# Kernel optimization log

Hardware: AMD Instinct MI355X
Metric: run time of the kernel (lower is better)

The kernel has to match this reference:

```python
import jax, jax.numpy as jnp
from jax import lax
import numpy as np


def conv2d(x, w, b):
    # x: NCHW, w: OIHW, VALID padding, stride 1
    y = lax.conv_general_dilated(x, w, (1, 1), 'VALID',
                                 dimension_numbers=('NCHW', 'OIHW', 'NCHW'))
    return y + b[None, :, None, None]


def prelu(x, a):
    # per-channel PReLU, a: (C,)
    return jnp.where(x >= 0, x, a[None, :, None, None] * x)


def maxpool_ceil(x, k, s):
    # max pool with ceil_mode=True: pad right/bottom with -inf as needed
    H, W = x.shape[2], x.shape[3]
    def pad_amt(n):
        out = -(-(n - k) // s) + 1  # ceil
        return max(0, (out - 1) * s + k - n)
    ph, pw = pad_amt(H), pad_amt(W)
    return lax.reduce_window(x, -jnp.inf, lax.max,
                             (1, 1, k, k), (1, 1, s, s),
                             ((0, 0), (0, 0), (0, ph), (0, pw)))


def setup_inputs() -> dict:
    key = jax.random.key(0)
    ks = jax.random.split(key, 24)
    N = 2048
    x = jax.random.normal(ks[0], (N, 3, 48, 48), dtype=jnp.float32)

    def w_init(k, shape, fan_in):
        return jax.random.normal(k, shape, dtype=jnp.float32) * (1.0 / np.sqrt(fan_in))

    inp = {'x': x}
    inp['c1w'] = w_init(ks[1], (32, 3, 3, 3), 3 * 9)
    inp['c1b'] = jnp.zeros((32,), jnp.float32)
    inp['a1'] = jax.random.uniform(ks[2], (32,), jnp.float32, 0.1, 0.4)
    inp['c2w'] = w_init(ks[3], (64, 32, 3, 3), 32 * 9)
    inp['c2b'] = jnp.zeros((64,), jnp.float32)
    inp['a2'] = jax.random.uniform(ks[4], (64,), jnp.float32, 0.1, 0.4)
    inp['c3w'] = w_init(ks[5], (64, 64, 3, 3), 64 * 9)
    inp['c3b'] = jnp.zeros((64,), jnp.float32)
    inp['a3'] = jax.random.uniform(ks[6], (64,), jnp.float32, 0.1, 0.4)
    inp['c4w'] = w_init(ks[7], (128, 64, 2, 2), 64 * 4)
    inp['c4b'] = jnp.zeros((128,), jnp.float32)
    inp['a4'] = jax.random.uniform(ks[8], (128,), jnp.float32, 0.1, 0.4)
    inp['d5w'] = w_init(ks[9], (256, 1152), 1152)
    inp['d5b'] = jnp.zeros((256,), jnp.float32)
    inp['a5'] = jax.random.uniform(ks[10], (256,), jnp.float32, 0.1, 0.4)
    inp['d61w'] = w_init(ks[11], (2, 256), 256)
    inp['d61b'] = jnp.zeros((2,), jnp.float32)
    inp['d62w'] = w_init(ks[12], (4, 256), 256)
    inp['d62b'] = jnp.zeros((4,), jnp.float32)
    inp['d63w'] = w_init(ks[13], (10, 256), 256)
    inp['d63b'] = jnp.zeros((10,), jnp.float32)
    return inp


def reference(x, c1w, c1b, a1, c2w, c2b, a2, c3w, c3b, a3, c4w, c4b, a4,
              d5w, d5b, a5, d61w, d61b, d62w, d62b, d63w, d63b):
    h = prelu(conv2d(x, c1w, c1b), a1)          # [N,32,46,46]
    h = maxpool_ceil(h, 3, 2)                   # [N,32,23,23]
    h = prelu(conv2d(h, c2w, c2b), a2)          # [N,64,21,21]
    h = maxpool_ceil(h, 3, 2)                   # [N,64,10,10]
    h = prelu(conv2d(h, c3w, c3b), a3)          # [N,64,8,8]
    h = maxpool_ceil(h, 2, 2)                   # [N,64,4,4]
    h = prelu(conv2d(h, c4w, c4b), a4)          # [N,128,3,3]
    # torch: x.permute(0,3,2,1).contiguous().view(N,-1)
    h = jnp.transpose(h, (0, 3, 2, 1)).reshape(h.shape[0], -1)  # [N,1152]
    h = h @ d5w.T + d5b                         # [N,256]
    h = jnp.where(h >= 0, h, a5 * h)            # PReLU over features
    a = jax.nn.softmax(h @ d61w.T + d61b, axis=1)  # class probs [N,2]
    b = h @ d62w.T + d62b
    c = h @ d63w.T + d63b                       # landmarks [N,10]
    return (b, c, a)
```

## Files before the change

### kernel.cpp

```cpp
#include <hip/hip_runtime.h>
#include <hip/hip_bf16.h>
#include <hip/hip_fp16.h>
#include <stdint.h>

typedef short s16x8 __attribute__((ext_vector_type(8)));
typedef unsigned short u16x8 __attribute__((ext_vector_type(8)));
typedef _Float16 f16x8 __attribute__((ext_vector_type(8)));
typedef float f32x4 __attribute__((ext_vector_type(4)));

__device__ __forceinline__ unsigned short f2bf(float f) {
    union { float f; unsigned u; } v; v.f = f;
    unsigned u = v.u;
    unsigned r = u + 0x7fffu + ((u >> 16) & 1u);
    return (unsigned short)(r >> 16);
}
__device__ __forceinline__ float bf2f(unsigned short h) {
    union { unsigned u; float f; } v; v.u = ((unsigned)h) << 16;
    return v.f;
}
__device__ __forceinline__ unsigned pkbf(float a, float b) {
    __hip_bfloat162 h = __float22bfloat162_rn(float2{a, b});
    union { __hip_bfloat162 h; unsigned u; } c; c.h = h; return c.u;
}
__device__ __forceinline__ float lo2f(unsigned d) {
    union { unsigned u; float f; } v; v.u = d << 16; return v.f;
}
__device__ __forceinline__ float hi2f(unsigned d) {
    union { unsigned u; float f; } v; v.u = d & 0xffff0000u; return v.f;
}
__device__ __forceinline__ unsigned short f2h(float f) {
    __half h = __float2half(f);
    union { __half h; unsigned short u; } c; c.h = h; return c.u;
}

__global__ void k0_prep(const float* __restrict__ c2w, const float* __restrict__ c3w,
                        const float* __restrict__ c4w, const float* __restrict__ d5w,
                        unsigned short* __restrict__ w2, unsigned short* __restrict__ w3,
                        unsigned short* __restrict__ w4, unsigned short* __restrict__ w5) {
    int t = blockIdx.x * 256 + threadIdx.x;
    if (t < 18432) {
        int kpos = t / 2048, rem = t % 2048, oc = rem / 32, ic = rem % 32;
        w2[t] = f2bf(c2w[(oc * 32 + ic) * 9 + kpos]);
        return;
    }
    t -= 18432;
    if (t < 36864) {
        int kpos = t / 4096, rem = t % 4096, oc = rem / 64, ic = rem % 64;
        w3[t] = f2bf(c3w[(oc * 64 + ic) * 9 + kpos]);
        return;
    }
    t -= 36864;
    if (t < 32768) {
        int kpos = t / 8192, rem = t % 8192, oc = rem / 64, ic = rem % 64;
        w4[t] = f2bf(c4w[(oc * 64 + ic) * 4 + kpos]);
        return;
    }
    t -= 32768;
    if (t < 294912) w5[t] = f2bf(d5w[t]);
}

__global__ __launch_bounds__(256, 6)
void k1_conv1(const float* __restrict__ x, const float* __restrict__ c1w,
              const float* __restrict__ c1b, const float* __restrict__ a1,
              unsigned short* __restrict__ p1) {
    __shared__ unsigned short xstrip[1008];
    __shared__ unsigned short cbuf[230 * 40];
    __shared__ unsigned short wlds[1024];
    __shared__ float bls[32], als[32];

    const int n = blockIdx.x, tid = threadIdx.x;
    const int w = tid >> 6, lane = tid & 63, q = lane >> 4, l16 = lane & 15;

    for (int t = tid; t < 1024; t += 256) {
        int oc = t >> 5, k = t & 31;
        wlds[t] = (k < 27) ? f2h(c1w[oc * 27 + k]) : (unsigned short)0;
    }
    if (tid < 32) { bls[tid] = c1b[tid]; als[tid] = a1[tid]; }
    __syncthreads();

    f16x8 Wf[2];
    #pragma unroll
    for (int nt = 0; nt < 2; ++nt) {
        union { u16x8 u; f16x8 f; } cc;
        cc.u = *(const u16x8*)(wlds + (nt * 16 + l16) * 32 + q * 8);
        Wf[nt] = cc.f;
    }

    float bq[2][4], aq[2][4];
    #pragma unroll
    for (int nt = 0; nt < 2; ++nt)
    #pragma unroll
    for (int r = 0; r < 4; ++r) {
        bq[nt][r] = bls[nt * 16 + q * 4 + r];
        aq[nt][r] = als[nt * 16 + q * 4 + r];
    }

    int off[8];
    #pragma unroll
    for (int j = 0; j < 8; ++j) {
        int k = q * 8 + j;
        int kk = k < 27 ? k : 26;
        int ic = kk / 9, r9 = kk - ic * 9, ky = r9 / 3, kx = r9 - ky * 3;
        off[j] = ic * 336 + ky * 48 + kx;
    }

    auto do_pool = [&](int sp, int nprows, int kymax) {
        int ntask = nprows * 92;
        int t = tid;
        if (t < ntask) {
            int ocg = t & 3; unsigned r2 = (unsigned)t >> 2;
            int px = (int)(r2 % 23u), py_l = (int)(r2 / 23u);
            int kxmax = (px == 22) ? 2 : 3;
            int base = (2 * py_l * 46 + 2 * px) * 40 + ocg * 8;
            float m0 = -3e38f, m1 = -3e38f, m2 = -3e38f, m3 = -3e38f;
            float m4 = -3e38f, m5 = -3e38f, m6 = -3e38f, m7 = -3e38f;
            #pragma unroll
            for (int ky = 0; ky < 3; ++ky) {
                if (ky < kymax) {
                    #pragma unroll
                    for (int kx = 0; kx < 3; ++kx) {
                        if (kx < kxmax) {
                            uint4 d = *(const uint4*)&cbuf[base + (ky * 46 + kx) * 40];
                            m0 = fmaxf(m0, lo2f(d.x)); m1 = fmaxf(m1, hi2f(d.x));
                            m2 = fmaxf(m2, lo2f(d.y)); m3 = fmaxf(m3, hi2f(d.y));
                            m4 = fmaxf(m4, lo2f(d.z)); m5 = fmaxf(m5, hi2f(d.z));
                            m6 = fmaxf(m6, lo2f(d.w)); m7 = fmaxf(m7, hi2f(d.w));
                        }
                    }
                }
            }
            uint4 ov;
            ov.x = pkbf(m0, m1); ov.y = pkbf(m2, m3);
            ov.z = pkbf(m4, m5); ov.w = pkbf(m6, m7);
            int py = 2 * sp + py_l;
            *(uint4*)&p1[n * 16928 + (py * 23 + px) * 32 + ocg * 8] = ov;
        }
    };

    for (int s = 0; s < 12; ++s) {
        const int nrows = (s == 11) ? 2 : 5;
        const int P = 46 * nrows;
        const int ntiles = (P + 15) >> 4;
        const int xr0 = 4 * s;

        {
            int t4 = tid;
            if (t4 < 252) {
                int ic = t4 / 84;
                int rem4 = t4 * 4 - ic * 336;
                int rr = rem4 / 48, col = rem4 - rr * 48;
                int row = xr0 + rr; if (row > 47) row = 47;
                float4 f = *(const float4*)(x + n * 6912 + ic * 2304 + row * 48 + col);
                ushort4 o;
                o.x = f2h(f.x); o.y = f2h(f.y); o.z = f2h(f.z); o.w = f2h(f.w);
                *(ushort4*)&xstrip[t4 * 4] = o;
            }
        }
        if (s > 0) do_pool(s - 1, 2, 3);
        __syncthreads();

        for (int T = w; T < ntiles; T += 4) {
            int px = T * 16 + l16;
            int p = px < P ? px : P - 1;
            int ry = p / 46, cx = p - ry * 46;
            int basex = ry * 48 + cx;
            union { u16x8 u; f16x8 f; } xcc;
            #pragma unroll
            for (int j = 0; j < 8; ++j) xcc.u[j] = xstrip[basex + off[j]];
            f16x8 Xf = xcc.f;
            f32x4 acc[2] = {{0.f,0.f,0.f,0.f},{0.f,0.f,0.f,0.f}};
            #pragma unroll
            for (int nt = 0; nt < 2; ++nt)
                acc[nt] = __builtin_amdgcn_mfma_f32_16x16x32_f16(Wf[nt], Xf, acc[nt], 0, 0, 0);
            if (px < P) {
                #pragma unroll
                for (int nt = 0; nt < 2; ++nt) {
                    float v0 = acc[nt][0] + bq[nt][0];
                    float v1 = acc[nt][1] + bq[nt][1];
                    float v2 = acc[nt][2] + bq[nt][2];
                    float v3 = acc[nt][3] + bq[nt][3];
                    v0 = fmaxf(v0, 0.f) + aq[nt][0] * fminf(v0, 0.f);
                    v1 = fmaxf(v1, 0.f) + aq[nt][1] * fminf(v1, 0.f);
                    v2 = fmaxf(v2, 0.f) + aq[nt][2] * fminf(v2, 0.f);
                    v3 = fmaxf(v3, 0.f) + aq[nt][3] * fminf(v3, 0.f);
                    uint2 pk; pk.x = pkbf(v0, v1); pk.y = pkbf(v2, v3);
                    *(uint2*)&cbuf[px * 40 + nt * 16 + q * 4] = pk;
                }
            }
        }
        __syncthreads();
    }
    do_pool(11, 1, 2);
}

__global__ __launch_bounds__(256, 2)
void k23_fused(const unsigned short* __restrict__ p1, const unsigned short* __restrict__ w2,
               const float* __restrict__ c2b, const float* __restrict__ a2,
               const unsigned short* __restrict__ w3, const float* __restrict__ c3b,
               const float* __restrict__ a3, const unsigned short* __restrict__ w4,
               const float* __restrict__ c4b, const float* __restrict__ a4,
               unsigned short* __restrict__ flat) {
    __shared__ __align__(16) char smem[52128];
    unsigned short* xs    = (unsigned short*)(smem);
    unsigned short* c2s   = (unsigned short*)(smem + 16560);
    unsigned short* p2s   = (unsigned short*)(smem + 37728);
    unsigned short* c3buf = (unsigned short*)(smem);
    unsigned short* p3    = (unsigned short*)(smem + 8192);

    const int n = blockIdx.x, tid = threadIdx.x;
    const int w = tid >> 6, lane = tid & 63, q = lane >> 4, l16 = lane & 15;
    const unsigned short* p1n = p1 + n * 16928;

    const int npair = w & 1, tset = w >> 1;
    const int ocA = npair * 32 + l16, ocB = npair * 32 + 16 + l16;

    s16x8 B2[9][2];
    #pragma unroll
    for (int kp = 0; kp < 9; ++kp) {
        B2[kp][0] = *(const s16x8*)(w2 + (kp * 64 + ocA) * 32 + q * 8);
        B2[kp][1] = *(const s16x8*)(w2 + (kp * 64 + ocB) * 32 + q * 8);
    }
    const float b2a = c2b[ocA], b2b = c2b[ocB];
    const float a2a = a2[ocA],  a2b = a2[ocB];

    auto stage = [&](int s) {
        int pr0 = 6 * s;
        for (int t = tid; t < 828; t += 256) {
            int pxl = t >> 2, c = t & 3;
            int rr = pxl / 23, colpx = pxl - rr * 23;
            int prow = pr0 + rr; if (prow > 22) prow = 22;
            uint4 d = ((const uint4*)p1n)[(prow * 23 + colpx) * 4 + c];
            ((uint4*)xs)[pxl * 5 + c] = d;
        }
    };

    auto conv2_strip = [&](int s) {
        const int nr = (s == 3) ? 3 : 7;
        const int P = 21 * nr;
        const int ntiles = (P + 15) >> 4;
        const int half = (ntiles + 1) >> 1;
        const int T0 = tset * half;
        const int T1 = (T0 + half) < ntiles ? (T0 + half) : ntiles;
        for (int T = T0; T < T1; ++T) {
            int m = T * 16 + l16;
            int p = m < P ? m : P - 1;
            int ry = p / 21, ox = p - ry * 21;
            const unsigned short* ab = xs + (ry * 23 + ox) * 40 + q * 8;
            f32x4 acc0 = {0.f, 0.f, 0.f, 0.f}, acc1 = {0.f, 0.f, 0.f, 0.f};
            #pragma unroll
            for (int kp = 0; kp < 9; ++kp) {
                int ky = kp / 3, kx = kp - ky * 3;
                s16x8 A = *(const s16x8*)(ab + (ky * 23 + kx) * 40);
                acc0 = __builtin_amdgcn_mfma_f32_16x16x32_bf16(A, B2[kp][0], acc0, 0, 0, 0);
                acc1 = __builtin_amdgcn_mfma_f32_16x16x32_bf16(A, B2[kp][1], acc1, 0, 0, 0);
            }
            int rowb = T * 16 + q * 4;
            #pragma unroll
            for (int r = 0; r < 4; ++r) {
                int row = rowb + r;
                if (row < P) {
                    float v0 = acc0[r] + b2a;
                    v0 = fmaxf(v0, 0.f) + a2a * fminf(v0, 0.f);
                    c2s[row * 72 + npair * 32 + l16] = f2bf(v0);
                    float v1 = acc1[r] + b2b;
                    v1 = fmaxf(v1, 0.f) + a2b * fminf(v1, 0.f);
                    c2s[row * 72 + npair * 32 + 16 + l16] = f2bf(v1);
                }
            }
        }
    };

    auto pool_strip = [&](int s) {
        int nprow = (s == 3) ? 1 : 3;
        int ntask = nprow * 80;
        if (tid < ntask) {
            int ocg = tid & 7; int r2 = tid >> 3;
            int px = r2 % 10, pyl = r2 / 10;
            int base = (2 * pyl * 21 + 2 * px) * 72 + ocg * 8;
            float m0 = -3e38f, m1 = -3e38f, m2 = -3e38f, m3 = -3e38f;
            float m4 = -3e38f, m5 = -3e38f, m6 = -3e38f, m7 = -3e38f;
            #pragma unroll
            for (int ky = 0; ky < 3; ++ky)
            #pragma unroll
            for (int kx = 0; kx < 3; ++kx) {
                uint4 d = *(const uint4*)&c2s[base + (ky * 21 + kx) * 72];
                m0 = fmaxf(m0, lo2f(d.x)); m1 = fmaxf(m1, hi2f(d.x));
                m2 = fmaxf(m2, lo2f(d.y)); m3 = fmaxf(m3, hi2f(d.y));
                m4 = fmaxf(m4, lo2f(d.z)); m5 = fmaxf(m5, hi2f(d.z));
                m6 = fmaxf(m6, lo2f(d.w)); m7 = fmaxf(m7, hi2f(d.w));
            }
            uint4 ov;
            ov.x = pkbf(m0, m1); ov.y = pkbf(m2, m3);
            ov.z = pkbf(m4, m5); ov.w = pkbf(m6, m7);
            *(uint4*)&p2s[((3 * s + pyl) * 10 + px) * 72 + ocg * 8] = ov;
        }
    };

    stage(0);
    __syncthreads();
    for (int s = 0; s < 4; ++s) {
        conv2_strip(s);
        __syncthreads();
        pool_strip(s);
        if (s < 3) stage(s + 1);
        __syncthreads();
    }

    {
        const int oc3 = w * 16 + l16;
        int mbase[4];
        #pragma unroll
        for (int j = 0; j < 4; ++j) {
            int px = j * 16 + l16;
            int oy = px >> 3, ox = px & 7;
            mbase[j] = (oy * 10 + ox) * 72 + q * 8;
        }
        f32x4 acc3[4];
        #pragma unroll
        for (int j = 0; j < 4; ++j) acc3[j] = f32x4{0.f, 0.f, 0.f, 0.f};
        s16x8 B3c = *(const s16x8*)(w3 + oc3 * 64 + q * 8);
        for (int c = 0; c < 18; ++c) {
            s16x8 B3n = B3c;
            if (c < 17) {
                int cn = c + 1;
                B3n = *(const s16x8*)(w3 + ((cn >> 1) * 64 + oc3) * 64 + (cn & 1) * 32 + q * 8);
            }
            int kp = c >> 1, ky = kp / 3, kx = kp - ky * 3;
            int aoff = (ky * 10 + kx) * 72 + (c & 1) * 32;
            #pragma unroll
            for (int j = 0; j < 4; ++j) {
                s16x8 A = *(const s16x8*)(p2s + mbase[j] + aoff);
                acc3[j] = __builtin_amdgcn_mfma_f32_16x16x32_bf16(A, B3c, acc3[j], 0, 0, 0);
            }
            B3c = B3n;
        }
        float bias = c3b[oc3], al = a3[oc3];
        #pragma unroll
        for (int j = 0; j < 4; ++j)
        #pragma unroll
        for (int r = 0; r < 4; ++r) {
            int row = j * 16 + q * 4 + r;
            float val = acc3[j][r] + bias;
            val = fmaxf(val, 0.f) + al * fminf(val, 0.f);
            c3buf[row * 64 + oc3] = f2bf(val);
        }
    }
    __syncthreads();

    for (int t = tid; t < 1024; t += 256) {
        int oc = t & 63, r = t >> 6, py = r >> 2, pxo = r & 3;
        float m = -3e38f;
        #pragma unroll
        for (int ky = 0; ky < 2; ++ky)
        #pragma unroll
        for (int kx = 0; kx < 2; ++kx)
            m = fmaxf(m, bf2f(c3buf[((py * 2 + ky) * 8 + pxo * 2 + kx) * 64 + oc]));
        p3[r * 72 + oc] = f2bf(m);
    }
    __syncthreads();

    {
        int px = l16 < 9 ? l16 : 8;
        int oy = px / 3, ox = px - oy * 3;
        const int mb4 = (oy * 4 + ox) * 72 + q * 8;
        const int oc4a = (w * 2) * 16 + l16, oc4b = (w * 2 + 1) * 16 + l16;
        f32x4 acc4[2] = {{0.f,0.f,0.f,0.f},{0.f,0.f,0.f,0.f}};
        s16x8 B4c[2];
        B4c[0] = *(const s16x8*)(w4 + oc4a * 64 + q * 8);
        B4c[1] = *(const s16x8*)(w4 + oc4b * 64 + q * 8);
        for (int c = 0; c < 8; ++c) {
            s16x8 B4n[2] = {B4c[0], B4c[1]};
            if (c < 7) {
                int cn = c + 1;
                int boff = (cn >> 1) * 8192 + (cn & 1) * 32 + q * 8;
                B4n[0] = *(const s16x8*)(w4 + boff + oc4a * 64);
                B4n[1] = *(const s16x8*)(w4 + boff + oc4b * 64);
            }
            int kp = c >> 1, ky = kp >> 1, kx = kp & 1;
            s16x8 A = *(const s16x8*)(p3 + mb4 + (ky * 4 + kx) * 72 + (c & 1) * 32);
            acc4[0] = __builtin_amdgcn_mfma_f32_16x16x32_bf16(A, B4c[0], acc4[0], 0, 0, 0);
            acc4[1] = __builtin_amdgcn_mfma_f32_16x16x32_bf16(A, B4c[1], acc4[1], 0, 0, 0);
            B4c[0] = B4n[0]; B4c[1] = B4n[1];
        }
        #pragma unroll
        for (int h = 0; h < 2; ++h) {
            int oc = h ? oc4b : oc4a;
            float bias = c4b[oc], al = a4[oc];
            #pragma unroll
            for (int r = 0; r < 4; ++r) {
                int row = q * 4 + r;
                if (row < 9) {
                    int hy = row / 3, wx = row - hy * 3;
                    float val = acc4[h][r] + bias;
                    val = fmaxf(val, 0.f) + al * fminf(val, 0.f);
                    flat[(unsigned)n * 1152u + (wx * 3 + hy) * 128 + oc] = f2bf(val);
                }
            }
        }
    }
}

__global__ __launch_bounds__(256, 2)
void k5a_gemm(const unsigned short* __restrict__ flat, const unsigned short* __restrict__ w5,
              const float* __restrict__ d5b, const float* __restrict__ a5,
              unsigned short* __restrict__ h) {
    __shared__ float hbuf[4 * 16 * 128];
    const int blk = blockIdx.x, tid = threadIdx.x;
    const int w = tid >> 6, lane = tid & 63, q = lane >> 4, l16 = lane & 15;
    const int img0 = (blk >> 1) * 16, ocb = (blk & 1) * 128;
    const int img = img0 + l16;

    f32x4 acc[8];
    #pragma unroll
    for (int nt = 0; nt < 8; ++nt) acc[nt] = f32x4{0.f, 0.f, 0.f, 0.f};

    for (int cc = 0; cc < 9; ++cc) {
        int c = w * 9 + cc;
        int k0 = c * 32 + q * 8;
        s16x8 A = *(const s16x8*)(flat + (unsigned)img * 1152u + k0);
        #pragma unroll
        for (int nt = 0; nt < 8; ++nt) {
            int oc = ocb + nt * 16 + l16;
            s16x8 B = *(const s16x8*)(w5 + (unsigned)oc * 1152u + k0);
            acc[nt] = __builtin_amdgcn_mfma_f32_16x16x32_bf16(A, B, acc[nt], 0, 0, 0);
        }
    }
    #pragma unroll
    for (int nt = 0; nt < 8; ++nt)
    #pragma unroll
    for (int r = 0; r < 4; ++r) {
        int row = q * 4 + r;
        hbuf[(w * 16 + row) * 128 + nt * 16 + l16] = acc[nt][r];
    }
    __syncthreads();
    for (int t = tid; t < 1024; t += 256) {
        int im = t >> 6, oc2 = (t & 63) * 2;
        float s0 = hbuf[im * 128 + oc2]        + hbuf[(16 + im) * 128 + oc2]
                 + hbuf[(32 + im) * 128 + oc2] + hbuf[(48 + im) * 128 + oc2];
        float s1 = hbuf[im * 128 + oc2 + 1]        + hbuf[(16 + im) * 128 + oc2 + 1]
                 + hbuf[(32 + im) * 128 + oc2 + 1] + hbuf[(48 + im) * 128 + oc2 + 1];
        int oc = ocb + oc2;
        s0 += d5b[oc];     s0 = fmaxf(s0, 0.f) + a5[oc] * fminf(s0, 0.f);
        s1 += d5b[oc + 1]; s1 = fmaxf(s1, 0.f) + a5[oc + 1] * fminf(s1, 0.f);
        *(unsigned*)&h[(unsigned)(img0 + im) * 256u + oc] = pkbf(s0, s1);
    }
}

__global__ __launch_bounds__(256, 2)
void k5b_head(const unsigned short* __restrict__ h,
              const float* __restrict__ d61w, const float* __restrict__ d61b,
              const float* __restrict__ d62w, const float* __restrict__ d62b,
              const float* __restrict__ d63w, const float* __restrict__ d63b,
              float* __restrict__ out) {
    __shared__ float hL[16 * 260];
    __shared__ float wl[16 * 260];
    __shared__ float lg[256];
    const int blk = blockIdx.x, tid = threadIdx.x;
    const int img0 = blk * 16;

    for (int t = tid; t < 512; t += 256) {
        int im = t >> 5, g = t & 31;
        uint4 d = *(const uint4*)&h[(unsigned)(img0 + im) * 256u + g * 8];
        float* dst = &hL[im * 260 + g * 8];
        dst[0] = lo2f(d.x); dst[1] = hi2f(d.x);
        dst[2] = lo2f(d.y); dst[3] = hi2f(d.y);
        dst[4] = lo2f(d.z); dst[5] = hi2f(d.z);
        dst[6] = lo2f(d.w); dst[7] = hi2f(d.w);
    }
    {
        int o = tid >> 4, seg = tid & 15;
        const float* wrow = (o < 2) ? d61w + o * 256
                          : (o < 6) ? d62w + (o - 2) * 256
                          :           d63w + (o - 6) * 256;
        #pragma unroll
        for (int j = 0; j < 4; ++j)
            *(float4*)&wl[o * 260 + seg * 16 + j * 4] = ((const float4*)wrow)[seg * 4 + j];
    }
    __syncthreads();

    const int im = tid >> 4, o = tid & 15;
    {
        float bias = (o < 2) ? d61b[o] : (o < 6) ? d62b[o - 2] : d63b[o - 6];
        float s = bias;
        const float4* ha = (const float4*)&hL[im * 260];
        const float4* wa = (const float4*)&wl[o * 260];
        #pragma unroll 8
        for (int k = 0; k < 64; ++k) {
            float4 a = ha[k], b = wa[k];
            s += a.x * b.x + a.y * b.y + a.z * b.z + a.w * b.w;
        }
        lg[im * 16 + o] = s;
    }
    __syncthreads();
    {
        int gimg = img0 + im;
        float v = lg[im * 16 + o];
        if (o >= 2 && o < 6) {
            out[gimg * 4 + (o - 2)] = v;
        } else if (o >= 6) {
            out[8192 + gimg * 10 + (o - 6)] = v;
        } else {
            float l0 = lg[im * 16 + 0], l1 = lg[im * 16 + 1];
            float mx = fmaxf(l0, l1);
            float e0 = __expf(l0 - mx), e1 = __expf(l1 - mx);
            out[28672 + gimg * 2 + o] = (o == 0 ? e0 : e1) / (e0 + e1);
        }
    }
}

extern "C" void kernel_launch(void* const* d_in, const int* in_sizes, int n_in,
                              void* d_out, int out_size, void* d_ws, size_t ws_size,
                              hipStream_t stream) {
    (void)in_sizes; (void)n_in; (void)out_size; (void)ws_size;
    const float* x    = (const float*)d_in[0];
    const float* c1w  = (const float*)d_in[1];
    const float* c1b  = (const float*)d_in[2];
    const float* a1   = (const float*)d_in[3];
    const float* c2w  = (const float*)d_in[4];
    const float* c2b  = (const float*)d_in[5];
    const float* a2   = (const float*)d_in[6];
    const float* c3w  = (const float*)d_in[7];
    const float* c3b  = (const float*)d_in[8];
    const float* a3   = (const float*)d_in[9];
    const float* c4w  = (const float*)d_in[10];
    const float* c4b  = (const float*)d_in[11];
    const float* a4   = (const float*)d_in[12];
    const float* d5w  = (const float*)d_in[13];
    const float* d5b  = (const float*)d_in[14];
    const float* a5   = (const float*)d_in[15];
    const float* d61w = (const float*)d_in[16];
    const float* d61b = (const float*)d_in[17];
    const float* d62w = (const float*)d_in[18];
    const float* d62b = (const float*)d_in[19];
    const float* d63w = (const float*)d_in[20];
    const float* d63b = (const float*)d_in[21];

    char* ws = (char*)d_ws;
    unsigned short* p1    = (unsigned short*)(ws + 0);
    unsigned short* flat  = (unsigned short*)(ws + 69337088);
    unsigned short* h     = (unsigned short*)(ws + 74055680);
    unsigned short* w2    = (unsigned short*)(ws + 186777600);
    unsigned short* w3    = (unsigned short*)(ws + 186814464);
    unsigned short* w4    = (unsigned short*)(ws + 186888192);
    unsigned short* w5    = (unsigned short*)(ws + 186953728);

    k0_prep  <<<1496, 256, 0, stream>>>(c2w, c3w, c4w, d5w, w2, w3, w4, w5);
    k1_conv1 <<<2048, 256, 0, stream>>>(x, c1w, c1b, a1, p1);
    k23_fused<<<2048, 256, 0, stream>>>(p1, w2, c2b, a2, w3, c3b, a3, w4, c4b, a4, flat);
    k5a_gemm <<<256, 256, 0, stream>>>(flat, w5, d5b, a5, h);
    k5b_head <<<128, 256, 0, stream>>>(h, d61w, d61b, d62w, d62b, d63w, d63b,
                                       (float*)d_out);
}
```

Baseline: 316.2 us.

## Switch intermediate activations and weights from bf16 to fp16 with packed max pooling

Result: faster. 296.9 us (-6.1%).

```diff
diff --git a/kernel.cpp b/kernel.cpp
--- a/kernel.cpp
+++ b/kernel.cpp
@@ -6,31 +6,20 @@
 typedef short s16x8 __attribute__((ext_vector_type(8)));
 typedef unsigned short u16x8 __attribute__((ext_vector_type(8)));
 typedef _Float16 f16x8 __attribute__((ext_vector_type(8)));
+typedef __fp16 h16x2 __attribute__((ext_vector_type(2)));
 typedef float f32x4 __attribute__((ext_vector_type(4)));
 
-__device__ __forceinline__ unsigned short f2bf(float f) {
-    union { float f; unsigned u; } v; v.f = f;
-    unsigned u = v.u;
-    unsigned r = u + 0x7fffu + ((u >> 16) & 1u);
-    return (unsigned short)(r >> 16);
-}
-__device__ __forceinline__ float bf2f(unsigned short h) {
-    union { unsigned u; float f; } v; v.u = ((unsigned)h) << 16;
-    return v.f;
-}
-__device__ __forceinline__ unsigned pkbf(float a, float b) {
-    __hip_bfloat162 h = __float22bfloat162_rn(float2{a, b});
-    union { __hip_bfloat162 h; unsigned u; } c; c.h = h; return c.u;
-}
-__device__ __forceinline__ float lo2f(unsigned d) {
-    union { unsigned u; float f; } v; v.u = d << 16; return v.f;
-}
-__device__ __forceinline__ float hi2f(unsigned d) {
-    union { unsigned u; float f; } v; v.u = d & 0xffff0000u; return v.f;
-}
 __device__ __forceinline__ unsigned short f2h(float f) {
     __half h = __float2half(f);
     union { __half h; unsigned short u; } c; c.h = h; return c.u;
+}
+__device__ __forceinline__ float h2f(unsigned short u) {
+    union { unsigned short u; __half h; } c; c.u = u; return __half2float(c.h);
+}
+__device__ __forceinline__ unsigned pkh(float a, float b) {
+    union { h16x2 h; unsigned u; } c;
+    c.h = __builtin_amdgcn_cvt_pkrtz(a, b);
+    return c.u;
 }
 
 __global__ void k0_prep(const float* __restrict__ c2w, const float* __restrict__ c3w,
@@ -40,23 +29,23 @@
     int t = blockIdx.x * 256 + threadIdx.x;
     if (t < 18432) {
         int kpos = t / 2048, rem = t % 2048, oc = rem / 32, ic = rem % 32;
-        w2[t] = f2bf(c2w[(oc * 32 + ic) * 9 + kpos]);
+        w2[t] = f2h(c2w[(oc * 32 + ic) * 9 + kpos]);
         return;
     }
     t -= 18432;
     if (t < 36864) {
         int kpos = t / 4096, rem = t % 4096, oc = rem / 64, ic = rem % 64;
-        w3[t] = f2bf(c3w[(oc * 64 + ic) * 9 + kpos]);
+        w3[t] = f2h(c3w[(oc * 64 + ic) * 9 + kpos]);
         return;
     }
     t -= 36864;
     if (t < 32768) {
         int kpos = t / 8192, rem = t % 8192, oc = rem / 64, ic = rem % 64;
-        w4[t] = f2bf(c4w[(oc * 64 + ic) * 4 + kpos]);
+        w4[t] = f2h(c4w[(oc * 64 + ic) * 4 + kpos]);
         return;
     }
     t -= 32768;
-    if (t < 294912) w5[t] = f2bf(d5w[t]);
+    if (t < 294912) w5[t] = f2h(d5w[t]);
 }
 
 __global__ __launch_bounds__(256, 6)
@@ -112,28 +101,25 @@
             int px = (int)(r2 % 23u), py_l = (int)(r2 / 23u);
             int kxmax = (px == 22) ? 2 : 3;
             int base = (2 * py_l * 46 + 2 * px) * 40 + ocg * 8;
-            float m0 = -3e38f, m1 = -3e38f, m2 = -3e38f, m3 = -3e38f;
-            float m4 = -3e38f, m5 = -3e38f, m6 = -3e38f, m7 = -3e38f;
+            f16x8 mx;
+            #pragma unroll
+            for (int j = 0; j < 8; ++j) mx[j] = (_Float16)(-60000.f);
             #pragma unroll
             for (int ky = 0; ky < 3; ++ky) {
                 if (ky < kymax) {
                     #pragma unroll
                     for (int kx = 0; kx < 3; ++kx) {
                         if (kx < kxmax) {
-                            uint4 d = *(const uint4*)&cbuf[base + (ky * 46 + kx) * 40];
-                            m0 = fmaxf(m0, lo2f(d.x)); m1 = fmaxf(m1, hi2f(d.x));
-                            m2 = fmaxf(m2, lo2f(d.y)); m3 = fmaxf(m3, hi2f(d.y));
-                            m4 = fmaxf(m4, lo2f(d.z)); m5 = fmaxf(m5, hi2f(d.z));
-                            m6 = fmaxf(m6, lo2f(d.w)); m7 = fmaxf(m7, hi2f(d.w));
+                            union { uint4 u; f16x8 f; } d;
+                            d.u = *(const uint4*)&cbuf[base + (ky * 46 + kx) * 40];
+                            mx = __builtin_elementwise_max(mx, d.f);
                         }
                     }
                 }
             }
-            uint4 ov;
-            ov.x = pkbf(m0, m1); ov.y = pkbf(m2, m3);
-            ov.z = pkbf(m4, m5); ov.w = pkbf(m6, m7);
+            union { f16x8 f; uint4 u; } o; o.f = mx;
             int py = 2 * sp + py_l;
-            *(uint4*)&p1[n * 16928 + (py * 23 + px) * 32 + ocg * 8] = ov;
+            *(uint4*)&p1[n * 16928 + (py * 23 + px) * 32 + ocg * 8] = o.u;
         }
     };
 
@@ -151,9 +137,8 @@
                 int rr = rem4 / 48, col = rem4 - rr * 48;
                 int row = xr0 + rr; if (row > 47) row = 47;
                 float4 f = *(const float4*)(x + n * 6912 + ic * 2304 + row * 48 + col);
-                ushort4 o;
-                o.x = f2h(f.x); o.y = f2h(f.y); o.z = f2h(f.z); o.w = f2h(f.w);
-                *(ushort4*)&xstrip[t4 * 4] = o;
+                uint2 o; o.x = pkh(f.x, f.y); o.y = pkh(f.z, f.w);
+                *(uint2*)&xstrip[t4 * 4] = o;
             }
         }
         if (s > 0) do_pool(s - 1, 2, 3);
@@ -183,7 +168,7 @@
                     v1 = fmaxf(v1, 0.f) + aq[nt][1] * fminf(v1, 0.f);
                     v2 = fmaxf(v2, 0.f) + aq[nt][2] * fminf(v2, 0.f);
                     v3 = fmaxf(v3, 0.f) + aq[nt][3] * fminf(v3, 0.f);
-                    uint2 pk; pk.x = pkbf(v0, v1); pk.y = pkbf(v2, v3);
+                    uint2 pk; pk.x = pkh(v0, v1); pk.y = pkh(v2, v3);
                     *(uint2*)&cbuf[px * 40 + nt * 16 + q * 4] = pk;
                 }
             }
@@ -214,11 +199,13 @@
     const int npair = w & 1, tset = w >> 1;
     const int ocA = npair * 32 + l16, ocB = npair * 32 + 16 + l16;
 
-    s16x8 B2[9][2];
+    f16x8 B2[9][2];
     #pragma unroll
     for (int kp = 0; kp < 9; ++kp) {
-        B2[kp][0] = *(const s16x8*)(w2 + (kp * 64 + ocA) * 32 + q * 8);
-        B2[kp][1] = *(const s16x8*)(w2 + (kp * 64 + ocB) * 32 + q * 8);
+        union { u16x8 u; f16x8 f; } c0, c1;
+        c0.u = *(const u16x8*)(w2 + (kp * 64 + ocA) * 32 + q * 8);
+        c1.u = *(const u16x8*)(w2 + (kp * 64 + ocB) * 32 + q * 8);
+        B2[kp][0] = c0.f; B2[kp][1] = c1.f;
     }
     const float b2a = c2b[ocA], b2b = c2b[ocB];
     const float a2a = a2[ocA],  a2b = a2[ocB];
@@ -250,9 +237,10 @@
             #pragma unroll
             for (int kp = 0; kp < 9; ++kp) {
                 int ky = kp / 3, kx = kp - ky * 3;
-                s16x8 A = *(const s16x8*)(ab + (ky * 23 + kx) * 40);
-                acc0 = __builtin_amdgcn_mfma_f32_16x16x32_bf16(A, B2[kp][0], acc0, 0, 0, 0);
-                acc1 = __builtin_amdgcn_mfma_f32_16x16x32_bf16(A, B2[kp][1], acc1, 0, 0, 0);
+                union { u16x8 u; f16x8 f; } av;
+                av.u = *(const u16x8*)(ab + (ky * 23 + kx) * 40);
+                acc0 = __builtin_amdgcn_mfma_f32_16x16x32_f16(av.f, B2[kp][0], acc0, 0, 0, 0);
+                acc1 = __builtin_amdgcn_mfma_f32_16x16x32_f16(av.f, B2[kp][1], acc1, 0, 0, 0);
             }
             int rowb = T * 16 + q * 4;
             #pragma unroll
@@ -261,10 +249,10 @@
                 if (row < P) {
                     float v0 = acc0[r] + b2a;
                     v0 = fmaxf(v0, 0.f) + a2a * fminf(v0, 0.f);
-                    c2s[row * 72 + npair * 32 + l16] = f2bf(v0);
+                    c2s[row * 72 + npair * 32 + l16] = f2h(v0);
                     float v1 = acc1[r] + b2b;
                     v1 = fmaxf(v1, 0.f) + a2b * fminf(v1, 0.f);
-                    c2s[row * 72 + npair * 32 + 16 + l16] = f2bf(v1);
+                    c2s[row * 72 + npair * 32 + 16 + l16] = f2h(v1);
                 }
             }
         }
@@ -277,22 +265,19 @@
             int ocg = tid & 7; int r2 = tid >> 3;
             int px = r2 % 10, pyl = r2 / 10;
             int base = (2 * pyl * 21 + 2 * px) * 72 + ocg * 8;
-            float m0 = -3e38f, m1 = -3e38f, m2 = -3e38f, m3 = -3e38f;
-            float m4 = -3e38f, m5 = -3e38f, m6 = -3e38f, m7 = -3e38f;
+            f16x8 mx;
+            #pragma unroll
+            for (int j = 0; j < 8; ++j) mx[j] = (_Float16)(-60000.f);
             #pragma unroll
             for (int ky = 0; ky < 3; ++ky)
             #pragma unroll
             for (int kx = 0; kx < 3; ++kx) {
-                uint4 d = *(const uint4*)&c2s[base + (ky * 21 + kx) * 72];
-                m0 = fmaxf(m0, lo2f(d.x)); m1 = fmaxf(m1, hi2f(d.x));
-                m2 = fmaxf(m2, lo2f(d.y)); m3 = fmaxf(m3, hi2f(d.y));
-                m4 = fmaxf(m4, lo2f(d.z)); m5 = fmaxf(m5, hi2f(d.z));
-                m6 = fmaxf(m6, lo2f(d.w)); m7 = fmaxf(m7, hi2f(d.w));
-            }
-            uint4 ov;
-            ov.x = pkbf(m0, m1); ov.y = pkbf(m2, m3);
-            ov.z = pkbf(m4, m5); ov.w = pkbf(m6, m7);
-            *(uint4*)&p2s[((3 * s + pyl) * 10 + px) * 72 + ocg * 8] = ov;
+                union { uint4 u; f16x8 f; } d;
+                d.u = *(const uint4*)&c2s[base + (ky * 21 + kx) * 72];
+                mx = __builtin_elementwise_max(mx, d.f);
+            }
+            union { f16x8 f; uint4 u; } o; o.f = mx;
+            *(uint4*)&p2s[((3 * s + pyl) * 10 + px) * 72 + ocg * 8] = o.u;
         }
     };
 
@@ -318,19 +303,24 @@
         f32x4 acc3[4];
         #pragma unroll
         for (int j = 0; j < 4; ++j) acc3[j] = f32x4{0.f, 0.f, 0.f, 0.f};
-        s16x8 B3c = *(const s16x8*)(w3 + oc3 * 64 + q * 8);
+        union { u16x8 u; f16x8 f; } bc;
+        bc.u = *(const u16x8*)(w3 + oc3 * 64 + q * 8);
+        f16x8 B3c = bc.f;
         for (int c = 0; c < 18; ++c) {
-            s16x8 B3n = B3c;
+            f16x8 B3n = B3c;
             if (c < 17) {
                 int cn = c + 1;
-                B3n = *(const s16x8*)(w3 + ((cn >> 1) * 64 + oc3) * 64 + (cn & 1) * 32 + q * 8);
+                union { u16x8 u; f16x8 f; } bn;
+                bn.u = *(const u16x8*)(w3 + ((cn >> 1) * 64 + oc3) * 64 + (cn & 1) * 32 + q * 8);
+                B3n = bn.f;
             }
             int kp = c >> 1, ky = kp / 3, kx = kp - ky * 3;
             int aoff = (ky * 10 + kx) * 72 + (c & 1) * 32;
             #pragma unroll
             for (int j = 0; j < 4; ++j) {
-                s16x8 A = *(const s16x8*)(p2s + mbase[j] + aoff);
-                acc3[j] = __builtin_amdgcn_mfma_f32_16x16x32_bf16(A, B3c, acc3[j], 0, 0, 0);
+                union { u16x8 u; f16x8 f; } av;
+                av.u = *(const u16x8*)(p2s + mbase[j] + aoff);
+                acc3[j] = __builtin_amdgcn_mfma_f32_16x16x32_f16(av.f, B3c, acc3[j], 0, 0, 0);
             }
             B3c = B3n;
         }
@@ -342,20 +332,27 @@
             int row = j * 16 + q * 4 + r;
             float val = acc3[j][r] + bias;
             val = fmaxf(val, 0.f) + al * fminf(val, 0.f);
-            c3buf[row * 64 + oc3] = f2bf(val);
-        }
-    }
-    __syncthreads();
-
-    for (int t = tid; t < 1024; t += 256) {
-        int oc = t & 63, r = t >> 6, py = r >> 2, pxo = r & 3;
-        float m = -3e38f;
+            c3buf[row * 64 + oc3] = f2h(val);
+        }
+    }
+    __syncthreads();
+
+    if (tid < 128) {
+        int ocg = tid & 7, r = tid >> 3;
+        int py = r >> 2, pxo = r & 3;
+        f16x8 mx;
+        #pragma unroll
+        for (int j = 0; j < 8; ++j) mx[j] = (_Float16)(-60000.f);
         #pragma unroll
         for (int ky = 0; ky < 2; ++ky)
         #pragma unroll
-        for (int kx = 0; kx < 2; ++kx)
-            m = fmaxf(m, bf2f(c3buf[((py * 2 + ky) * 8 + pxo * 2 + kx) * 64 + oc]));
-        p3[r * 72 + oc] = f2bf(m);
+        for (int kx = 0; kx < 2; ++kx) {
+            union { uint4 u; f16x8 f; } d;
+            d.u = *(const uint4*)&c3buf[((py * 2 + ky) * 8 + pxo * 2 + kx) * 64 + ocg * 8];
+            mx = __builtin_elementwise_max(mx, d.f);
+        }
+        union { f16x8 f; uint4 u; } o; o.f = mx;
+        *(uint4*)&p3[r * 72 + ocg * 8] = o.u;
     }
     __syncthreads();
 
@@ -365,21 +362,28 @@
         const int mb4 = (oy * 4 + ox) * 72 + q * 8;
         const int oc4a = (w * 2) * 16 + l16, oc4b = (w * 2 + 1) * 16 + l16;
         f32x4 acc4[2] = {{0.f,0.f,0.f,0.f},{0.f,0.f,0.f,0.f}};
-        s16x8 B4c[2];
-        B4c[0] = *(const s16x8*)(w4 + oc4a * 64 + q * 8);
-        B4c[1] = *(const s16x8*)(w4 + oc4b * 64 + q * 8);
+        f16x8 B4c[2];
+        {
+            union { u16x8 u; f16x8 f; } b0, b1;
+            b0.u = *(const u16x8*)(w4 + oc4a * 64 + q * 8);
+            b1.u = *(const u16x8*)(w4 + oc4b * 64 + q * 8);
+            B4c[0] = b0.f; B4c[1] = b1.f;
+        }
         for (int c = 0; c < 8; ++c) {
-            s16x8 B4n[2] = {B4c[0], B4c[1]};
+            f16x8 B4n[2] = {B4c[0], B4c[1]};
             if (c < 7) {
                 int cn = c + 1;
                 int boff = (cn >> 1) * 8192 + (cn & 1) * 32 + q * 8;
-                B4n[0] = *(const s16x8*)(w4 + boff + oc4a * 64);
-                B4n[1] = *(const s16x8*)(w4 + boff + oc4b * 64);
+                union { u16x8 u; f16x8 f; } b0, b1;
+                b0.u = *(const u16x8*)(w4 + boff + oc4a * 64);
+                b1.u = *(const u16x8*)(w4 + boff + oc4b * 64);
+                B4n[0] = b0.f; B4n[1] = b1.f;
             }
             int kp = c >> 1, ky = kp >> 1, kx = kp & 1;
-            s16x8 A = *(const s16x8*)(p3 + mb4 + (ky * 4 + kx) * 72 + (c & 1) * 32);
-            acc4[0] = __builtin_amdgcn_mfma_f32_16x16x32_bf16(A, B4c[0], acc4[0], 0, 0, 0);
-            acc4[1] = __builtin_amdgcn_mfma_f32_16x16x32_bf16(A, B4c[1], acc4[1], 0, 0, 0);
+            union { u16x8 u; f16x8 f; } av;
+            av.u = *(const u16x8*)(p3 + mb4 + (ky * 4 + kx) * 72 + (c & 1) * 32);
+            acc4[0] = __builtin_amdgcn_mfma_f32_16x16x32_f16(av.f, B4c[0], acc4[0], 0, 0, 0);
+            acc4[1] = __builtin_amdgcn_mfma_f32_16x16x32_f16(av.f, B4c[1], acc4[1], 0, 0, 0);
             B4c[0] = B4n[0]; B4c[1] = B4n[1];
         }
         #pragma unroll
@@ -393,7 +397,7 @@
                     int hy = row / 3, wx = row - hy * 3;
                     float val = acc4[h][r] + bias;
                     val = fmaxf(val, 0.f) + al * fminf(val, 0.f);
-                    flat[(unsigned)n * 1152u + (wx * 3 + hy) * 128 + oc] = f2bf(val);
+                    flat[(unsigned)n * 1152u + (wx * 3 + hy) * 128 + oc] = f2h(val);
                 }
             }
         }
@@ -417,12 +421,14 @@
     for (int cc = 0; cc < 9; ++cc) {
         int c = w * 9 + cc;
         int k0 = c * 32 + q * 8;
-        s16x8 A = *(const s16x8*)(flat + (unsigned)img * 1152u + k0);
+        union { u16x8 u; f16x8 f; } av;
+        av.u = *(const u16x8*)(flat + (unsigned)img * 1152u + k0);
         #pragma unroll
         for (int nt = 0; nt < 8; ++nt) {
             int oc = ocb + nt * 16 + l16;
-            s16x8 B = *(const s16x8*)(w5 + (unsigned)oc * 1152u + k0);
-            acc[nt] = __builtin_amdgcn_mfma_f32_16x16x32_bf16(A, B, acc[nt], 0, 0, 0);
+            union { u16x8 u; f16x8 f; } bv;
+            bv.u = *(const u16x8*)(w5 + (unsigned)oc * 1152u + k0);
+            acc[nt] = __builtin_amdgcn_mfma_f32_16x16x32_f16(av.f, bv.f, acc[nt], 0, 0, 0);
         }
     }
     #pragma unroll
@@ -442,7 +448,7 @@
         int oc = ocb + oc2;
         s0 += d5b[oc];     s0 = fmaxf(s0, 0.f) + a5[oc] * fminf(s0, 0.f);
         s1 += d5b[oc + 1]; s1 = fmaxf(s1, 0.f) + a5[oc + 1] * fminf(s1, 0.f);
-        *(unsigned*)&h[(unsigned)(img0 + im) * 256u + oc] = pkbf(s0, s1);
+        *(unsigned*)&h[(unsigned)(img0 + im) * 256u + oc] = pkh(s0, s1);
     }
 }
 
@@ -460,12 +466,11 @@
 
     for (int t = tid; t < 512; t += 256) {
         int im = t >> 5, g = t & 31;
-        uint4 d = *(const uint4*)&h[(unsigned)(img0 + im) * 256u + g * 8];
+        union { uint4 u; f16x8 f; } d;
+        d.u = *(const uint4*)&h[(unsigned)(img0 + im) * 256u + g * 8];
         float* dst = &hL[im * 260 + g * 8];
-        dst[0] = lo2f(d.x); dst[1] = hi2f(d.x);
-        dst[2] = lo2f(d.y); dst[3] = hi2f(d.y);
-        dst[4] = lo2f(d.z); dst[5] = hi2f(d.z);
-        dst[6] = lo2f(d.w); dst[7] = hi2f(d.w);
+        #pragma unroll
+        for (int j = 0; j < 8; ++j) dst[j] = (float)d.f[j];
     }
     {
         int o = tid >> 4, seg = tid & 15;
```
